# Kernel optimization log

Measured on AMD Instinct MI355X. Metric: run time of the kernel, lower is better.

Reference implementation:

```python
import jax, jax.numpy as jnp
import numpy as np

N, E, G = 50000, 1600000, 500
H, F, NG, L, OUT = 128, 128, 50, 6, 1
LOG2 = float(np.log(2.0))

def ssp(x):
    return jax.nn.softplus(x) - LOG2

def setup_inputs() -> dict:
    key = jax.random.key(0)
    ks = jax.random.split(key, 16)
    inp = {
        'z': jax.random.randint(ks[0], (N,), 0, 100),
        'pos': jax.random.normal(ks[1], (N, 3), jnp.float32) * 5.0,
        'batch': jnp.sort(jax.random.randint(ks[2], (N,), 0, G)),
        'edge_index': jax.random.randint(ks[3], (2, E), 0, N),
        # parameters
        'emb': jax.random.normal(ks[4], (100, H), jnp.float32) * 0.1,
        'dist_W': jax.random.normal(ks[5], (1, NG), jnp.float32) * 0.1,
        'dist_b': jnp.zeros((NG,), jnp.float32),
        'Wn': jax.random.normal(ks[6], (L, H, F), jnp.float32) * (1.0 / np.sqrt(H)),
        'We': jax.random.normal(ks[7], (L, NG, F), jnp.float32) * (1.0 / np.sqrt(NG)),
        'be': jnp.zeros((L, F), jnp.float32),
        'Wo': jax.random.normal(ks[8], (L, F, H), jnp.float32) * (1.0 / np.sqrt(F)),
        'bo': jnp.zeros((L, H), jnp.float32),
        'W1': jax.random.normal(ks[9], (H, H // 2), jnp.float32) * (1.0 / np.sqrt(H)),
        'b1': jnp.zeros((H // 2,), jnp.float32),
        'W2': jax.random.normal(ks[10], (H // 2, OUT), jnp.float32) * (1.0 / np.sqrt(H // 2)),
        'b2': jnp.zeros((OUT,), jnp.float32),
    }
    return inp

def reference(z, pos, batch, edge_index, emb, dist_W, dist_b, Wn, We, be, Wo, bo, W1, b1, W2, b2):
    row, col = edge_index[0], edge_index[1]
    # edge distances -> Linear(1, num_gaussians)
    dist = jnp.linalg.norm(pos[row] - pos[col], axis=-1)            # [E]
    e = dist[:, None] * dist_W[0][None, :] + dist_b                 # [E, NG]
    v = emb[z]                                                      # [N, H]
    # edge-conditioned message passing x num_layers
    for i in range(Wn.shape[0]):
        h = v @ Wn[i]                                               # [N, F]
        msg = h[col] * (e @ We[i] + be[i])                          # [E, F]
        agg = jax.ops.segment_sum(msg, row, num_segments=v.shape[0])
        v = ssp(agg @ Wo[i] + bo[i])                                # [N, H]
    # readout
    u = ssp(v @ W1 + b1) @ W2 + b2                                  # [N, OUT]
    return jax.ops.segment_sum(u, batch, num_segments=G)            # [G, OUT]
```

## Files before the change

kernel.cpp:

```cpp
#include <hip/hip_runtime.h>
#include <math.h>

#define HDIM 128
#define NGAUSS 50
#define NLAYER 6
#define TSTR 136
#define DINV (1.0f/512.0f)
#define NXCD 8
#define NSTRIPE 512

typedef unsigned short ushortT;
typedef __attribute__((ext_vector_type(8))) short bf16x8;
typedef __attribute__((ext_vector_type(4))) float f32x4;

static __device__ __forceinline__ float bf2f(unsigned short u){
  union { unsigned int i; float f; } x; x.i = ((unsigned int)u) << 16; return x.f;
}
static __device__ __forceinline__ float bitsf(unsigned int i){
  union { unsigned int i; float f; } x; x.i = i; return x.f;
}
static __device__ __forceinline__ unsigned short f2bf(float f){
  union { float f; unsigned int i; } x; x.f = f;
  unsigned int i = x.i;
  unsigned int r = (i + 0x7FFFu + ((i >> 16) & 1u)) >> 16;
  return (unsigned short)r;
}
static __device__ __forceinline__ float ssp(float x){
  return fmaxf(x, 0.0f) + __logf(1.0f + __expf(-fabsf(x))) - 0.69314718055994530942f;
}
static __device__ __forceinline__ f32x4 mfma4r(const bf16x8* a, const bf16x8* b){
  f32x4 d = {0.f, 0.f, 0.f, 0.f};
  d = __builtin_amdgcn_mfma_f32_16x16x32_bf16(a[0], b[0], d, 0, 0, 0);
  d = __builtin_amdgcn_mfma_f32_16x16x32_bf16(a[1], b[1], d, 0, 0, 0);
  d = __builtin_amdgcn_mfma_f32_16x16x32_bf16(a[2], b[2], d, 0, 0, 0);
  d = __builtin_amdgcn_mfma_f32_16x16x32_bf16(a[3], b[3], d, 0, 0, 0);
  return d;
}


__global__ __launch_bounds__(256)
void k_hist(const int* __restrict__ erow, int* __restrict__ hist,
            int E, int NB, int shift, int estripe){
  __shared__ int lh[512];
  int tid = threadIdx.x, w = blockIdx.x;
  for (int i = tid; i < NB; i += 256) lh[i] = 0;
  __syncthreads();
  int beg = w * estripe;
  int end = beg + estripe; if (end > E) end = E;
  for (int e = beg + tid; e < end; e += 256)
    atomicAdd(&lh[erow[e] >> shift], 1);
  __syncthreads();
  for (int i = tid; i < NB; i += 256) hist[w * 512 + i] = lh[i];
}

__global__ __launch_bounds__(256)
void k_colscan(int* __restrict__ hist, int* __restrict__ colTotal, int NB){
  __shared__ int sA[512], sB[512];
  int b = blockIdx.x, tid = threadIdx.x;
  sA[tid]       = hist[tid * 512 + b];
  sA[tid + 256] = hist[(tid + 256) * 512 + b];
  __syncthreads();
  int* pa = sA; int* pb = sB;
  for (int off = 1; off < 512; off <<= 1){
    for (int i = tid; i < 512; i += 256)
      pb[i] = pa[i] + (i >= off ? pa[i - off] : 0);
    __syncthreads();
    int* t = pa; pa = pb; pb = t;
  }
  int e0 = (tid == 0) ? 0 : pa[tid - 1];
  int e1 = pa[tid + 255];
  hist[tid * 512 + b]       = e0;
  hist[(tid + 256) * 512 + b] = e1;
  if (tid == 0) colTotal[b] = pa[511];
}

__global__ __launch_bounds__(256)
void k_bscan(const int* __restrict__ colTotal, int* __restrict__ bucketBase, int NB){
  __shared__ int sA[512], sB[512];
  int tid = threadIdx.x;
  for (int i = tid; i < 512; i += 256) sA[i] = (i < NB) ? colTotal[i] : 0;
  __syncthreads();
  int* pa = sA; int* pb = sB;
  for (int off = 1; off < 512; off <<= 1){
    for (int i = tid; i < 512; i += 256)
      pb[i] = pa[i] + (i >= off ? pa[i - off] : 0);
    __syncthreads();
    int* t = pa; pa = pb; pb = t;
  }
  for (int i = tid; i < NB; i += 256)
    bucketBase[i] = (i == 0) ? 0 : pa[i - 1];
  if (tid == 0) bucketBase[NB] = pa[NB - 1];
}

__global__ __launch_bounds__(256)
void k_scatter(const int* __restrict__ erow, const int* __restrict__ ecol,
               const float* __restrict__ pos, const int* __restrict__ hist,
               const int* __restrict__ bucketBase, uint2* __restrict__ stg,
               int E, int NB, int shift, int estripe){
  __shared__ int cur[512];
  int tid = threadIdx.x, w = blockIdx.x;
  for (int b = tid; b < NB; b += 256)
    cur[b] = bucketBase[b] + hist[w * 512 + b];
  __syncthreads();
  int beg = w * estripe;
  int end = beg + estripe; if (end > E) end = E;
  int mask = (1 << shift) - 1;
  for (int e = beg + tid; e < end; e += 256){
    int r = erow[e], c = ecol[e];
    float dx = pos[r*3+0] - pos[c*3+0];
    float dy = pos[r*3+1] - pos[c*3+1];
    float dz = pos[r*3+2] - pos[c*3+2];
    float d = sqrtf(dx*dx + dy*dy + dz*dz);
    int du = (int)(d * 512.0f + 0.5f);
    if (du > 65535) du = 65535;
    int p = atomicAdd(&cur[r >> shift], 1);
    uint2 t;
    t.x = ((unsigned int)c << 16) | (unsigned int)du;
    t.y = (unsigned int)(r & mask);
    stg[p] = t;
  }
}

__global__ __launch_bounds__(256)
void k_place(const uint2* __restrict__ stg, const int* __restrict__ bucketBase,
             int* __restrict__ offsets, unsigned int* __restrict__ csr,
             int N, int NB, int shift, int E){
  __shared__ int rc[1024];
  __shared__ int sA[1024], sB[1024];
  int b = blockIdx.x, tid = threadIdx.x;
  int R = 1 << shift;
  int r0 = b << shift;
  int s = bucketBase[b], e2 = bucketBase[b + 1];
  for (int i = tid; i < R; i += 256) rc[i] = 0;
  __syncthreads();
  for (int j = s + tid; j < e2; j += 256)
    atomicAdd(&rc[stg[j].y], 1);
  __syncthreads();
  for (int i = tid; i < R; i += 256) sA[i] = rc[i];
  __syncthreads();
  int* pa = sA; int* pb = sB;
  for (int off = 1; off < R; off <<= 1){
    for (int i = tid; i < R; i += 256)
      pb[i] = pa[i] + (i >= off ? pa[i - off] : 0);
    __syncthreads();
    int* t = pa; pa = pb; pb = t;
  }
  for (int i = tid; i < R; i += 256){
    int excl = (i == 0) ? 0 : pa[i - 1];
    rc[i] = excl;
    int r = r0 + i;
    if (r < N) offsets[r] = s + excl;
  }
  if (b == NB - 1 && tid == 0) offsets[N] = E;
  __syncthreads();
  for (int j = s + tid; j < e2; j += 256){
    uint2 t = stg[j];
    int slot = s + atomicAdd(&rc[t.y], 1);
    csr[slot] = t.x;
  }
}

__global__ void k_setup(const int* __restrict__ z, const float* __restrict__ emb,
                        ushortT* __restrict__ vhi,
                        const float* __restrict__ Wn, ushortT* __restrict__ WnT,
                        const float* __restrict__ Wo, ushortT* __restrict__ WoT,
                        const float* __restrict__ dW, const float* __restrict__ db,
                        const float* __restrict__ We, const float* __restrict__ be,
                        float* __restrict__ a, float* __restrict__ c,
                        const int* __restrict__ batch, int* __restrict__ groupOff,
                        const float* __restrict__ W1, ushortT* __restrict__ W1T,
                        int N, int G, int B1, int B2, int B4, int B5, int B7){
  int b = blockIdx.x;
  int tid = threadIdx.x;
  if (b < B1){
    int idx = b * 256 + tid;
    if (idx < N * HDIM){
      int n = idx >> 7, f = idx & 127;
      vhi[idx] = f2bf(emb[z[n] * HDIM + f]);
    }
    return;
  }
  b -= B1;
  if (b < B2){
    int idx = b * 256 + tid;
    if (idx < NLAYER * HDIM * HDIM){
      int mat = idx >> 14, rem = idx & 16383;
      int n = rem >> 7, k = rem & 127;
      WnT[idx] = f2bf(Wn[(mat << 14) + k * HDIM + n]);
    }
    return;
  }
  b -= B2;
  if (b < B2){
    int idx = b * 256 + tid;
    if (idx < NLAYER * HDIM * HDIM){
      int mat = idx >> 14, rem = idx & 16383;
      int n = rem >> 7, k = rem & 127;
      WoT[idx] = f2bf(Wo[(mat << 14) + k * HDIM + n]);
    }
    return;
  }
  b -= B2;
  if (b < B4){
    int idx = b * 256 + tid;
    if (idx < NLAYER * HDIM){
      int l = idx >> 7, f = idx & 127;
      float av = 0.f, cv = 0.f;
      for (int g = 0; g < NGAUSS; ++g){
        float we = We[(l * NGAUSS + g) * HDIM + f];
        av += dW[g] * we;
        cv += db[g] * we;
      }
      a[idx] = av;
      c[idx] = cv + be[idx];
    }
    return;
  }
  b -= B4;
  if (b < B5){
    int i = b * 256 + tid;
    if (i >= N) return;
    int bb = batch[i];
    if (i == 0){
      for (int g = 0; g <= bb; ++g) groupOff[g] = 0;
    } else {
      int pb = batch[i - 1];
      for (int g = pb + 1; g <= bb; ++g) groupOff[g] = i;
    }
    if (i == N - 1){
      for (int g = bb + 1; g <= G; ++g) groupOff[g] = N;
    }
    return;
  }
  b -= B5;
  if (b < B7){
    int idx = b * 256 + tid;
    if (idx < 64 * HDIM){
      int ncol = idx >> 7, k = idx & 127;
      W1T[idx] = f2bf(W1[k * 64 + ncol]);
    }
  }
}

__global__ __launch_bounds__(128, 2)
void k_gemm0(const ushortT* __restrict__ X, const ushortT* __restrict__ WT,
             ushortT* __restrict__ outHi, int N){
  int tid = threadIdx.x;
  int wave = tid >> 6, lane = tid & 63;
  int m = lane & 15, quad = lane >> 4;
  int ntiles = (N + 15) >> 4;
  int t0 = (blockIdx.x * 2 + wave) * 2;
  if (t0 >= ntiles) return;

  bf16x8 av[2][4];
  #pragma unroll
  for (int rt = 0; rt < 2; ++rt){
    int row = (t0 + rt) * 16 + m; if (row >= N) row = N - 1;
    #pragma unroll
    for (int kk = 0; kk < 4; ++kk)
      av[rt][kk] = *(const bf16x8*)(X + ((size_t)row << 7) + kk*32 + quad*8);
  }
  #pragma unroll
  for (int ct = 0; ct < 8; ++ct){
    int ncol = ct * 16 + m;
    const ushortT* bp = WT + ((size_t)ncol << 7) + quad*8;
    bf16x8 bb[4];
    #pragma unroll
    for (int kk = 0; kk < 4; ++kk) bb[kk] = *(const bf16x8*)(bp + kk*32);
    #pragma unroll
    for (int rt = 0; rt < 2; ++rt){
      f32x4 d = mfma4r(av[rt], bb);
      #pragma unroll
      for (int r = 0; r < 4; ++r){
        int orow = (t0 + rt) * 16 + quad*4 + r;
        if (orow < N) outHi[((size_t)orow << 7) + ncol] = f2bf(d[r]);
      }
    }
  }
}

#define AGG_PROC(P, DD) do { \
    unsigned int w_; float lo_, hi_; \
    w_ = (P).x; lo_ = bitsf(w_ << 16); hi_ = bitsf(w_ & 0xFFFF0000u); \
    s1[0] = fmaf(lo_, (DD), s1[0]); s0[0] += lo_; \
    s1[1] = fmaf(hi_, (DD), s1[1]); s0[1] += hi_; \
    w_ = (P).y; lo_ = bitsf(w_ << 16); hi_ = bitsf(w_ & 0xFFFF0000u); \
    s1[2] = fmaf(lo_, (DD), s1[2]); s0[2] += lo_; \
    s1[3] = fmaf(hi_, (DD), s1[3]); s0[3] += hi_; \
    w_ = (P).z; lo_ = bitsf(w_ << 16); hi_ = bitsf(w_ & 0xFFFF0000u); \
    s1[4] = fmaf(lo_, (DD), s1[4]); s0[4] += lo_; \
    s1[5] = fmaf(hi_, (DD), s1[5]); s0[5] += hi_; \
    w_ = (P).w; lo_ = bitsf(w_ << 16); hi_ = bitsf(w_ & 0xFFFF0000u); \
    s1[6] = fmaf(lo_, (DD), s1[6]); s0[6] += lo_; \
    s1[7] = fmaf(hi_, (DD), s1[7]); s0[7] += hi_; \
  } while(0)

#define GATH(Q) (*(const uint4*)(h + ((size_t)((Q) >> 16) << 7) + fl))

__global__ __launch_bounds__(256, 6)
void k_agg2(const ushortT* __restrict__ h, const int* __restrict__ offsets,
            const unsigned int* __restrict__ cd, const float* __restrict__ a,
            const float* __restrict__ c, ushortT* __restrict__ aggHi,
            int N, int segNodes){
  int xcd = blockIdx.x & (NXCD - 1);
  int idx = blockIdx.x >> 3;
  int node = xcd * segNodes + idx * 4 + (threadIdx.x >> 6);
  if (node >= N || node >= (xcd + 1) * segNodes) return;
  int lane = threadIdx.x & 63;
  int quarter = lane >> 4;
  int fl = (lane & 15) * 8;
  int s = offsets[node], e = offsets[node + 1];
  float s0[8] = {0.f,0.f,0.f,0.f,0.f,0.f,0.f,0.f};
  float s1[8] = {0.f,0.f,0.f,0.f,0.f,0.f,0.f,0.f};
  int efull = s + ((e - s) & ~7);
  int L = s;
  if (efull - s >= 16){
    unsigned int qA0 = cd[L + quarter],      qA1 = cd[L + 4 + quarter];
    uint4 pA0 = GATH(qA0), pA1 = GATH(qA1);
    unsigned int qB0 = cd[L + 8 + quarter],  qB1 = cd[L + 12 + quarter];
    uint4 pB0 = GATH(qB0), pB1 = GATH(qB1);
    float dA0 = (float)(qA0 & 0xFFFFu) * DINV, dA1 = (float)(qA1 & 0xFFFFu) * DINV;
    float dB0 = (float)(qB0 & 0xFFFFu) * DINV, dB1 = (float)(qB1 & 0xFFFFu) * DINV;
    L += 16;
    for (; L + 16 <= efull; L += 16){
      unsigned int nA0 = cd[L + quarter], nA1 = cd[L + 4 + quarter];
      AGG_PROC(pA0, dA0); AGG_PROC(pA1, dA1);
      pA0 = GATH(nA0); pA1 = GATH(nA1);
      dA0 = (float)(nA0 & 0xFFFFu) * DINV; dA1 = (float)(nA1 & 0xFFFFu) * DINV;
      unsigned int nB0 = cd[L + 8 + quarter], nB1 = cd[L + 12 + quarter];
      AGG_PROC(pB0, dB0); AGG_PROC(pB1, dB1);
      pB0 = GATH(nB0); pB1 = GATH(nB1);
      dB0 = (float)(nB0 & 0xFFFFu) * DINV; dB1 = (float)(nB1 & 0xFFFFu) * DINV;
    }
    AGG_PROC(pA0, dA0); AGG_PROC(pA1, dA1);
    AGG_PROC(pB0, dB0); AGG_PROC(pB1, dB1);
  }
  for (; L + 8 <= efull; L += 8){
    unsigned int q0 = cd[L + quarter], q1 = cd[L + 4 + quarter];
    uint4 p0 = GATH(q0), p1 = GATH(q1);
    float d0 = (float)(q0 & 0xFFFFu) * DINV, d1 = (float)(q1 & 0xFFFFu) * DINV;
    AGG_PROC(p0, d0); AGG_PROC(p1, d1);
  }
  for (int j = efull; j < e; j += 4){
    int myj = j + quarter;
    if (myj < e){
      unsigned int q = cd[myj];
      uint4 p = GATH(q);
      float dd = (float)(q & 0xFFFFu) * DINV;
      AGG_PROC(p, dd);
    }
  }
  float4 av0 = *(const float4*)(a + fl);
  float4 av1 = *(const float4*)(a + fl + 4);
  float4 cv0 = *(const float4*)(c + fl);
  float4 cv1 = *(const float4*)(c + fl + 4);
  float r[8];
  r[0] = av0.x * s1[0] + cv0.x * s0[0];
  r[1] = av0.y * s1[1] + cv0.y * s0[1];
  r[2] = av0.z * s1[2] + cv0.z * s0[2];
  r[3] = av0.w * s1[3] + cv0.w * s0[3];
  r[4] = av1.x * s1[4] + cv1.x * s0[4];
  r[5] = av1.y * s1[5] + cv1.y * s0[5];
  r[6] = av1.z * s1[6] + cv1.z * s0[6];
  r[7] = av1.w * s1[7] + cv1.w * s0[7];
  #pragma unroll
  for (int k = 0; k < 8; ++k){
    r[k] += __shfl_down(r[k], 32, 64);
    r[k] += __shfl_down(r[k], 16, 64);
  }
  if (quarter == 0){
    uint4 st;
    st.x = (unsigned int)f2bf(r[0]) | ((unsigned int)f2bf(r[1]) << 16);
    st.y = (unsigned int)f2bf(r[2]) | ((unsigned int)f2bf(r[3]) << 16);
    st.z = (unsigned int)f2bf(r[4]) | ((unsigned int)f2bf(r[5]) << 16);
    st.w = (unsigned int)f2bf(r[6]) | ((unsigned int)f2bf(r[7]) << 16);
    *(uint4*)(aggHi + ((size_t)node << 7) + fl) = st;
  }
}

__global__ __launch_bounds__(256, 2)
void k_fpair(const ushortT* __restrict__ agg, const ushortT* __restrict__ WoT,
             const float* __restrict__ bo, const ushortT* __restrict__ WnT,
             ushortT* __restrict__ outH, int N, int segTiles){
  __shared__ ushortT vt[2][32 * TSTR];
  int tid = threadIdx.x;
  int wave = tid >> 6, lane = tid & 63;
  int pairI = wave >> 1, half = wave & 1;
  int m = lane & 15, quad = lane >> 4;
  int ntiles = (N + 15) >> 4;
  int xcd = blockIdx.x & (NXCD - 1);
  int idx = blockIdx.x >> 3;
  int wjIdx = idx * 2 + pairI;
  int segWJ = segTiles >> 1;
  int t0 = xcd * segTiles + wjIdx * 2;
  bool act = (wjIdx < segWJ) && (t0 < ntiles);
  ushortT* vw = vt[pairI];

  bf16x8 av[2][4];
  if (act){
    #pragma unroll
    for (int rt = 0; rt < 2; ++rt){
      int row = (t0 + rt) * 16 + m; if (row >= N) row = N - 1;
      #pragma unroll
      for (int kk = 0; kk < 4; ++kk)
        av[rt][kk] = *(const bf16x8*)(agg + ((size_t)row << 7) + kk*32 + quad*8);
    }
    #pragma unroll
    for (int cti = 0; cti < 4; ++cti){
      int ncol = (half * 4 + cti) * 16 + m;
      const ushortT* bp = WoT + ((size_t)ncol << 7) + quad*8;
      bf16x8 bb[4];
      #pragma unroll
      for (int kk = 0; kk < 4; ++kk) bb[kk] = *(const bf16x8*)(bp + kk*32);
      float bbias = bo[ncol];
      #pragma unroll
      for (int rt = 0; rt < 2; ++rt){
        f32x4 d = mfma4r(av[rt], bb);
        #pragma unroll
        for (int r = 0; r < 4; ++r)
          vw[(rt*16 + quad*4 + r) * TSTR + ncol] = f2bf(ssp(d[r] + bbias));
      }
    }
  }
  __syncthreads();
  if (act){
    bf16x8 a2[2][4];
    #pragma unroll
    for (int rt = 0; rt < 2; ++rt){
      #pragma unroll
      for (int kk = 0; kk < 4; ++kk)
        a2[rt][kk] = *(const bf16x8*)(&vw[(rt*16 + m) * TSTR + kk*32 + quad*8]);
    }
    #pragma unroll
    for (int cti = 0; cti < 4; ++cti){
      int ncol = (half * 4 + cti) * 16 + m;
      const ushortT* bp = WnT + ((size_t)ncol << 7) + quad*8;
      bf16x8 bb[4];
      #pragma unroll
      for (int kk = 0; kk < 4; ++kk) bb[kk] = *(const bf16x8*)(bp + kk*32);
      #pragma unroll
      for (int rt = 0; rt < 2; ++rt){
        f32x4 d = mfma4r(a2[rt], bb);
        #pragma unroll
        for (int r = 0; r < 4; ++r){
          int orow = (t0 + rt) * 16 + quad*4 + r;
          if (orow < N) outH[((size_t)orow << 7) + ncol] = f2bf(d[r]);
        }
      }
    }
  }
}

__global__ __launch_bounds__(256, 2)
void k_gfinal(const ushortT* __restrict__ agg, const ushortT* __restrict__ WoT,
              const float* __restrict__ bo, const ushortT* __restrict__ W1T,
              const float* __restrict__ b1, const float* __restrict__ W2,
              const float* __restrict__ b2, float* __restrict__ u,
              int N, int segTiles){
  __shared__ ushortT vt[2][32 * TSTR];
  __shared__ float part[2][2][32];
  int tid = threadIdx.x;
  int wave = tid >> 6, lane = tid & 63;
  int pairI = wave >> 1, half = wave & 1;
  int m = lane & 15, quad = lane >> 4;
  int ntiles = (N + 15) >> 4;
  int xcd = blockIdx.x & (NXCD - 1);
  int idx = blockIdx.x >> 3;
  int wjIdx = idx * 2 + pairI;
  int segWJ = segTiles >> 1;
  int t0 = xcd * segTiles + wjIdx * 2;
  bool act = (wjIdx < segWJ) && (t0 < ntiles);
  ushortT* vw = vt[pairI];

  if (act){
    bf16x8 av[2][4];
    #pragma unroll
    for (int rt = 0; rt < 2; ++rt){
      int row = (t0 + rt) * 16 + m; if (row >= N) row = N - 1;
      #pragma unroll
      for (int kk = 0; kk < 4; ++kk)
        av[rt][kk] = *(const bf16x8*)(agg + ((size_t)row << 7) + kk*32 + quad*8);
    }
    #pragma unroll
    for (int cti = 0; cti < 4; ++cti){
      int ncol = (half * 4 + cti) * 16 + m;
      const ushortT* bp = WoT + ((size_t)ncol << 7) + quad*8;
      bf16x8 bb[4];
      #pragma unroll
      for (int kk = 0; kk < 4; ++kk) bb[kk] = *(const bf16x8*)(bp + kk*32);
      float bbias = bo[ncol];
      #pragma unroll
      for (int rt = 0; rt < 2; ++rt){
        f32x4 d = mfma4r(av[rt], bb);
        #pragma unroll
        for (int r = 0; r < 4; ++r)
          vw[(rt*16 + quad*4 + r) * TSTR + ncol] = f2bf(ssp(d[r] + bbias));
      }
    }
  }
  __syncthreads();
  if (act){
    bf16x8 a2[2][4];
    #pragma unroll
    for (int rt = 0; rt < 2; ++rt){
      #pragma unroll
      for (int kk = 0; kk < 4; ++kk)
        a2[rt][kk] = *(const bf16x8*)(&vw[(rt*16 + m) * TSTR + kk*32 + quad*8]);
    }
    float acc[2][4] = {{0.f,0.f,0.f,0.f},{0.f,0.f,0.f,0.f}};
    #pragma unroll
    for (int cti = 0; cti < 2; ++cti){
      int ncol = (half * 2 + cti) * 16 + m;
      const ushortT* bp = W1T + ((size_t)ncol << 7) + quad*8;
      bf16x8 bb[4];
      #pragma unroll
      for (int kk = 0; kk < 4; ++kk) bb[kk] = *(const bf16x8*)(bp + kk*32);
      float bb1 = b1[ncol];
      float w2  = W2[ncol];
      #pragma unroll
      for (int rt = 0; rt < 2; ++rt){
        f32x4 d = mfma4r(a2[rt], bb);
        #pragma unroll
        for (int r = 0; r < 4; ++r)
          acc[rt][r] += ssp(d[r] + bb1) * w2;
      }
    }
    #pragma unroll
    for (int rt = 0; rt < 2; ++rt){
      #pragma unroll
      for (int r = 0; r < 4; ++r){
        float v = acc[rt][r];
        v += __shfl_xor(v, 1, 64);
        v += __shfl_xor(v, 2, 64);
        v += __shfl_xor(v, 4, 64);
        v += __shfl_xor(v, 8, 64);
        if (m == 0) part[pairI][half][rt*16 + quad*4 + r] = v;
      }
    }
  }
  __syncthreads();
  if (tid < 64){
    int p = tid >> 5, row = tid & 31;
    int wj = idx * 2 + p;
    int tt = xcd * segTiles + wj * 2;
    if (wj < segWJ && tt < ntiles){
      int orow = tt * 16 + row;
      if (orow < N) u[orow] = part[p][0][row] + part[p][1][row] + b2[0];
    }
  }
}

__global__ void k_gsum(const float* __restrict__ u, const int* __restrict__ groupOff,
                       float* __restrict__ out, int G){
  int g = blockIdx.x * 4 + (threadIdx.x >> 6);
  if (g >= G) return;
  int lane = threadIdx.x & 63;
  int s = groupOff[g], e = groupOff[g + 1];
  float acc = 0.f;
  for (int j = s + lane; j < e; j += 64) acc += u[j];
  #pragma unroll
  for (int off = 32; off > 0; off >>= 1)
    acc += __shfl_down(acc, off, 64);
  if (lane == 0) out[g] = acc;
}

extern "C" void kernel_launch(void* const* d_in, const int* in_sizes, int n_in,
                              void* d_out, int out_size, void* d_ws, size_t ws_size,
                              hipStream_t stream){
  const int N = in_sizes[0];
  const int E = in_sizes[3] / 2;
  const int G = out_size;

  const int*   z     = (const int*)d_in[0];
  const float* pos   = (const float*)d_in[1];
  const int*   batch = (const int*)d_in[2];
  const int*   eidx  = (const int*)d_in[3];
  const int*   erow  = eidx;
  const int*   ecol  = eidx + E;
  const float* emb   = (const float*)d_in[4];
  const float* dW    = (const float*)d_in[5];
  const float* db    = (const float*)d_in[6];
  const float* Wn    = (const float*)d_in[7];
  const float* We    = (const float*)d_in[8];
  const float* be    = (const float*)d_in[9];
  const float* Wo    = (const float*)d_in[10];
  const float* bo    = (const float*)d_in[11];
  const float* W1    = (const float*)d_in[12];
  const float* b1    = (const float*)d_in[13];
  const float* W2    = (const float*)d_in[14];
  const float* b2    = (const float*)d_in[15];

  char* ws = (char*)d_ws;
  size_t off = 0;
  auto alloc = [&](size_t bytes) -> char* {
    char* p = ws + off;
    off = (off + bytes + 255) & ~(size_t)255;
    return p;
  };
  size_t hbytes = (size_t)N * HDIM * 2;
  size_t stgbytes = (size_t)E * 8;
  int*          offsets  = (int*)         alloc((size_t)(N + 1) * 4);
  unsigned int* csr      = (unsigned int*)alloc((size_t)E * 4);
  ushortT*      h0       = (ushortT*)     alloc(hbytes);
  ushortT*      h1       = (ushortT*)     alloc(hbytes);
  ushortT*      vhi      = (ushortT*)     alloc(hbytes);
  ushortT*      agghi    = (ushortT*)     alloc(hbytes);
  ushortT*      stgbuf   = (ushortT*)     alloc(stgbytes);
  ushortT*      WnT      = (ushortT*)     alloc((size_t)NLAYER * HDIM * HDIM * 2);
  ushortT*      WoT      = (ushortT*)     alloc((size_t)NLAYER * HDIM * HDIM * 2);
  ushortT*      W1T      = (ushortT*)     alloc((size_t)64 * HDIM * 2);
  float*        a        = (float*)       alloc((size_t)NLAYER * HDIM * 4);
  float*        c        = (float*)       alloc((size_t)NLAYER * HDIM * 4);
  float*        u        = (float*)       alloc((size_t)N * 4);
  int*          groupOff = (int*)         alloc((size_t)(G + 1) * 4);

  int*   hist       = (int*)h1;
  int*   colTotal   = hist + NSTRIPE * 512;
  int*   bucketBase = colTotal + 512;
  uint2* stg        = (uint2*)stgbuf;

  int shift = 7;
  while ((((N - 1) >> shift) + 1) > 512) ++shift;
  int NB = ((N - 1) >> shift) + 1;
  int estripe = (E + NSTRIPE - 1) / NSTRIPE;

  int B1 = (N * HDIM + 255) / 256;
  int B2 = (NLAYER * HDIM * HDIM + 255) / 256;
  int B4 = (NLAYER * HDIM + 255) / 256;
  int B5 = (N + 255) / 256;
  int B7 = (64 * HDIM + 255) / 256;
  k_setup<<<B1 + 2*B2 + B4 + B5 + B7, 256, 0, stream>>>(
      z, emb, vhi, Wn, WnT, Wo, WoT,
      dW, db, We, be, a, c, batch, groupOff, W1, W1T,
      N, G, B1, B2, B4, B5, B7);

  k_hist   <<<NSTRIPE, 256, 0, stream>>>(erow, hist, E, NB, shift, estripe);
  k_colscan<<<NB,      256, 0, stream>>>(hist, colTotal, NB);
  k_bscan  <<<1,       256, 0, stream>>>(colTotal, bucketBase, NB);
  k_scatter<<<NSTRIPE, 256, 0, stream>>>(erow, ecol, pos, hist, bucketBase,
                                         stg, E, NB, shift, estripe);
  k_place  <<<NB,      256, 0, stream>>>(stg, bucketBase, offsets, csr, N, NB, shift, E);

  int ntiles = (N + 15) >> 4;
  int segTiles = (((ntiles + NXCD - 1) / NXCD) + 1) & ~1;
  int segNodes = segTiles * 16;
  int segWJ = segTiles >> 1;
  int aggGrid  = NXCD * ((segNodes + 3) / 4);
  int gGrid    = NXCD * ((segWJ + 1) / 2);
  int nwj = (ntiles + 1) / 2;
  int pairGrid = (nwj + 1) / 2;
  k_gemm0<<<pairGrid, 128, 0, stream>>>(vhi, WnT, h0, N);

  for (int l = 0; l < NLAYER; ++l){
    size_t wo = (size_t)l * HDIM * HDIM;
    const ushortT* hin  = (l & 1) ? h1 : h0;
    ushortT*       hout = (l & 1) ? h0 : h1;
    k_agg2<<<aggGrid, 256, 0, stream>>>(hin, offsets, csr,
                                        a + l * HDIM, c + l * HDIM, agghi, N, segNodes);
    if (l < NLAYER - 1){
      size_t wn = (size_t)(l + 1) * HDIM * HDIM;
      k_fpair<<<gGrid, 256, 0, stream>>>(agghi, WoT + wo, bo + (size_t)l * HDIM,
                                         WnT + wn, hout, N, segTiles);
    } else {
      k_gfinal<<<gGrid, 256, 0, stream>>>(agghi, WoT + wo, bo + (size_t)l * HDIM,
                                          W1T, b1, W2, b2, u, N, segTiles);
    }
  }
  k_gsum<<<(G + 3) / 4, 256, 0, stream>>>(u, groupOff, (float*)d_out, G);
}
```

Before: 582.5 us.

## Precompute embedding times Wn0 table, fuse histogram into setup, pack agg FMAs

The first-layer node projection is now computed once on a 100-row embedding table (emb@Wn[0]) and gathered per node, which removes the N×128×128 gemm0 kernel and the vhi buffer. The edge histogram kernel is folded into k_setup as extra blocks, saving a launch. The aggregation inner loop switches to 2-wide float vectors so the compiler can emit packed FMA/add instructions. The new path also rounds emb@Wn to bf16 in a slightly different order, which risks small numeric differences.

```diff
diff --git a/kernel.cpp b/kernel.cpp
--- a/kernel.cpp
+++ b/kernel.cpp
@@ -12,6 +12,7 @@
 typedef unsigned short ushortT;
 typedef __attribute__((ext_vector_type(8))) short bf16x8;
 typedef __attribute__((ext_vector_type(4))) float f32x4;
+typedef __attribute__((ext_vector_type(2))) float f32x2;
 
 static __device__ __forceinline__ float bf2f(unsigned short u){
   union { unsigned int i; float f; } x; x.i = ((unsigned int)u) << 16; return x.f;
@@ -37,21 +38,6 @@
   return d;
 }
 
-
-__global__ __launch_bounds__(256)
-void k_hist(const int* __restrict__ erow, int* __restrict__ hist,
-            int E, int NB, int shift, int estripe){
-  __shared__ int lh[512];
-  int tid = threadIdx.x, w = blockIdx.x;
-  for (int i = tid; i < NB; i += 256) lh[i] = 0;
-  __syncthreads();
-  int beg = w * estripe;
-  int end = beg + estripe; if (end > E) end = E;
-  for (int e = beg + tid; e < end; e += 256)
-    atomicAdd(&lh[erow[e] >> shift], 1);
-  __syncthreads();
-  for (int i = tid; i < NB; i += 256) hist[w * 512 + i] = lh[i];
-}
 
 __global__ __launch_bounds__(256)
 void k_colscan(int* __restrict__ hist, int* __restrict__ colTotal, int NB){
@@ -160,8 +146,21 @@
   }
 }
 
-__global__ void k_setup(const int* __restrict__ z, const float* __restrict__ emb,
-                        ushortT* __restrict__ vhi,
+__global__ __launch_bounds__(256)
+void k_emb2(const float* __restrict__ emb, const float* __restrict__ Wn,
+            ushortT* __restrict__ emb2){
+  int idx = blockIdx.x * 256 + threadIdx.x;
+  if (idx >= 100 * HDIM) return;
+  int i = idx >> 7, f = idx & 127;
+  float acc = 0.f;
+  #pragma unroll 8
+  for (int k = 0; k < HDIM; ++k)
+    acc = fmaf(emb[i * HDIM + k], Wn[k * HDIM + f], acc);
+  emb2[idx] = f2bf(acc);
+}
+
+__global__ void k_setup(const int* __restrict__ z, const ushortT* __restrict__ emb2,
+                        ushortT* __restrict__ h0,
                         const float* __restrict__ Wn, ushortT* __restrict__ WnT,
                         const float* __restrict__ Wo, ushortT* __restrict__ WoT,
                         const float* __restrict__ dW, const float* __restrict__ db,
@@ -169,14 +168,17 @@
                         float* __restrict__ a, float* __restrict__ c,
                         const int* __restrict__ batch, int* __restrict__ groupOff,
                         const float* __restrict__ W1, ushortT* __restrict__ W1T,
-                        int N, int G, int B1, int B2, int B4, int B5, int B7){
+                        const int* __restrict__ erow, int* __restrict__ hist,
+                        int N, int G, int E, int estripe, int NB, int shift,
+                        int B1, int B2, int B4, int B5, int B7){
+  __shared__ int lh[512];
   int b = blockIdx.x;
   int tid = threadIdx.x;
   if (b < B1){
     int idx = b * 256 + tid;
     if (idx < N * HDIM){
       int n = idx >> 7, f = idx & 127;
-      vhi[idx] = f2bf(emb[z[n] * HDIM + f]);
+      h0[idx] = emb2[z[n] * HDIM + f];
     }
     return;
   }
@@ -239,60 +241,32 @@
       int ncol = idx >> 7, k = idx & 127;
       W1T[idx] = f2bf(W1[k * 64 + ncol]);
     }
-  }
-}
-
-__global__ __launch_bounds__(128, 2)
-void k_gemm0(const ushortT* __restrict__ X, const ushortT* __restrict__ WT,
-             ushortT* __restrict__ outHi, int N){
-  int tid = threadIdx.x;
-  int wave = tid >> 6, lane = tid & 63;
-  int m = lane & 15, quad = lane >> 4;
-  int ntiles = (N + 15) >> 4;
-  int t0 = (blockIdx.x * 2 + wave) * 2;
-  if (t0 >= ntiles) return;
-
-  bf16x8 av[2][4];
-  #pragma unroll
-  for (int rt = 0; rt < 2; ++rt){
-    int row = (t0 + rt) * 16 + m; if (row >= N) row = N - 1;
-    #pragma unroll
-    for (int kk = 0; kk < 4; ++kk)
-      av[rt][kk] = *(const bf16x8*)(X + ((size_t)row << 7) + kk*32 + quad*8);
-  }
-  #pragma unroll
-  for (int ct = 0; ct < 8; ++ct){
-    int ncol = ct * 16 + m;
-    const ushortT* bp = WT + ((size_t)ncol << 7) + quad*8;
-    bf16x8 bb[4];
-    #pragma unroll
-    for (int kk = 0; kk < 4; ++kk) bb[kk] = *(const bf16x8*)(bp + kk*32);
-    #pragma unroll
-    for (int rt = 0; rt < 2; ++rt){
-      f32x4 d = mfma4r(av[rt], bb);
-      #pragma unroll
-      for (int r = 0; r < 4; ++r){
-        int orow = (t0 + rt) * 16 + quad*4 + r;
-        if (orow < N) outHi[((size_t)orow << 7) + ncol] = f2bf(d[r]);
-      }
-    }
-  }
-}
-
-#define AGG_PROC(P, DD) do { \
-    unsigned int w_; float lo_, hi_; \
-    w_ = (P).x; lo_ = bitsf(w_ << 16); hi_ = bitsf(w_ & 0xFFFF0000u); \
-    s1[0] = fmaf(lo_, (DD), s1[0]); s0[0] += lo_; \
-    s1[1] = fmaf(hi_, (DD), s1[1]); s0[1] += hi_; \
-    w_ = (P).y; lo_ = bitsf(w_ << 16); hi_ = bitsf(w_ & 0xFFFF0000u); \
-    s1[2] = fmaf(lo_, (DD), s1[2]); s0[2] += lo_; \
-    s1[3] = fmaf(hi_, (DD), s1[3]); s0[3] += hi_; \
-    w_ = (P).z; lo_ = bitsf(w_ << 16); hi_ = bitsf(w_ & 0xFFFF0000u); \
-    s1[4] = fmaf(lo_, (DD), s1[4]); s0[4] += lo_; \
-    s1[5] = fmaf(hi_, (DD), s1[5]); s0[5] += hi_; \
-    w_ = (P).w; lo_ = bitsf(w_ << 16); hi_ = bitsf(w_ & 0xFFFF0000u); \
-    s1[6] = fmaf(lo_, (DD), s1[6]); s0[6] += lo_; \
-    s1[7] = fmaf(hi_, (DD), s1[7]); s0[7] += hi_; \
+    return;
+  }
+  b -= B7;
+  if (b < NSTRIPE){
+    for (int i = tid; i < NB; i += 256) lh[i] = 0;
+    __syncthreads();
+    int beg = b * estripe;
+    int end = beg + estripe; if (end > E) end = E;
+    for (int e = beg + tid; e < end; e += 256)
+      atomicAdd(&lh[erow[e] >> shift], 1);
+    __syncthreads();
+    for (int i = tid; i < NB; i += 256) hist[b * 512 + i] = lh[i];
+  }
+}
+
+#define SPLAT(x) (f32x2){(x),(x)}
+#define AGG_PROC(P, DDV) do { \
+    unsigned int w_; f32x2 hv_; \
+    w_ = (P).x; hv_.x = bitsf(w_ << 16); hv_.y = bitsf(w_ & 0xFFFF0000u); \
+    s1v0 = __builtin_elementwise_fma(hv_, (DDV), s1v0); s0v0 += hv_; \
+    w_ = (P).y; hv_.x = bitsf(w_ << 16); hv_.y = bitsf(w_ & 0xFFFF0000u); \
+    s1v1 = __builtin_elementwise_fma(hv_, (DDV), s1v1); s0v1 += hv_; \
+    w_ = (P).z; hv_.x = bitsf(w_ << 16); hv_.y = bitsf(w_ & 0xFFFF0000u); \
+    s1v2 = __builtin_elementwise_fma(hv_, (DDV), s1v2); s0v2 += hv_; \
+    w_ = (P).w; hv_.x = bitsf(w_ << 16); hv_.y = bitsf(w_ & 0xFFFF0000u); \
+    s1v3 = __builtin_elementwise_fma(hv_, (DDV), s1v3); s0v3 += hv_; \
   } while(0)
 
 #define GATH(Q) (*(const uint4*)(h + ((size_t)((Q) >> 16) << 7) + fl))
@@ -310,8 +284,8 @@
   int quarter = lane >> 4;
   int fl = (lane & 15) * 8;
   int s = offsets[node], e = offsets[node + 1];
-  float s0[8] = {0.f,0.f,0.f,0.f,0.f,0.f,0.f,0.f};
-  float s1[8] = {0.f,0.f,0.f,0.f,0.f,0.f,0.f,0.f};
+  f32x2 s0v0 = {0.f,0.f}, s0v1 = {0.f,0.f}, s0v2 = {0.f,0.f}, s0v3 = {0.f,0.f};
+  f32x2 s1v0 = {0.f,0.f}, s1v1 = {0.f,0.f}, s1v2 = {0.f,0.f}, s1v3 = {0.f,0.f};
   int efull = s + ((e - s) & ~7);
   int L = s;
   if (efull - s >= 16){
@@ -319,18 +293,22 @@
     uint4 pA0 = GATH(qA0), pA1 = GATH(qA1);
     unsigned int qB0 = cd[L + 8 + quarter],  qB1 = cd[L + 12 + quarter];
     uint4 pB0 = GATH(qB0), pB1 = GATH(qB1);
-    float dA0 = (float)(qA0 & 0xFFFFu) * DINV, dA1 = (float)(qA1 & 0xFFFFu) * DINV;
-    float dB0 = (float)(qB0 & 0xFFFFu) * DINV, dB1 = (float)(qB1 & 0xFFFFu) * DINV;
+    f32x2 dA0 = SPLAT((float)(qA0 & 0xFFFFu) * DINV);
+    f32x2 dA1 = SPLAT((float)(qA1 & 0xFFFFu) * DINV);
+    f32x2 dB0 = SPLAT((float)(qB0 & 0xFFFFu) * DINV);
+    f32x2 dB1 = SPLAT((float)(qB1 & 0xFFFFu) * DINV);
     L += 16;
     for (; L + 16 <= efull; L += 16){
       unsigned int nA0 = cd[L + quarter], nA1 = cd[L + 4 + quarter];
       AGG_PROC(pA0, dA0); AGG_PROC(pA1, dA1);
       pA0 = GATH(nA0); pA1 = GATH(nA1);
-      dA0 = (float)(nA0 & 0xFFFFu) * DINV; dA1 = (float)(nA1 & 0xFFFFu) * DINV;
+      dA0 = SPLAT((float)(nA0 & 0xFFFFu) * DINV);
+      dA1 = SPLAT((float)(nA1 & 0xFFFFu) * DINV);
       unsigned int nB0 = cd[L + 8 + quarter], nB1 = cd[L + 12 + quarter];
       AGG_PROC(pB0, dB0); AGG_PROC(pB1, dB1);
       pB0 = GATH(nB0); pB1 = GATH(nB1);
-      dB0 = (float)(nB0 & 0xFFFFu) * DINV; dB1 = (float)(nB1 & 0xFFFFu) * DINV;
+      dB0 = SPLAT((float)(nB0 & 0xFFFFu) * DINV);
+      dB1 = SPLAT((float)(nB1 & 0xFFFFu) * DINV);
     }
     AGG_PROC(pA0, dA0); AGG_PROC(pA1, dA1);
     AGG_PROC(pB0, dB0); AGG_PROC(pB1, dB1);
@@ -338,7 +316,8 @@
   for (; L + 8 <= efull; L += 8){
     unsigned int q0 = cd[L + quarter], q1 = cd[L + 4 + quarter];
     uint4 p0 = GATH(q0), p1 = GATH(q1);
-    float d0 = (float)(q0 & 0xFFFFu) * DINV, d1 = (float)(q1 & 0xFFFFu) * DINV;
+    f32x2 d0 = SPLAT((float)(q0 & 0xFFFFu) * DINV);
+    f32x2 d1 = SPLAT((float)(q1 & 0xFFFFu) * DINV);
     AGG_PROC(p0, d0); AGG_PROC(p1, d1);
   }
   for (int j = efull; j < e; j += 4){
@@ -346,7 +325,7 @@
     if (myj < e){
       unsigned int q = cd[myj];
       uint4 p = GATH(q);
-      float dd = (float)(q & 0xFFFFu) * DINV;
+      f32x2 dd = SPLAT((float)(q & 0xFFFFu) * DINV);
       AGG_PROC(p, dd);
     }
   }
@@ -355,14 +334,14 @@
   float4 cv0 = *(const float4*)(c + fl);
   float4 cv1 = *(const float4*)(c + fl + 4);
   float r[8];
-  r[0] = av0.x * s1[0] + cv0.x * s0[0];
-  r[1] = av0.y * s1[1] + cv0.y * s0[1];
-  r[2] = av0.z * s1[2] + cv0.z * s0[2];
-  r[3] = av0.w * s1[3] + cv0.w * s0[3];
-  r[4] = av1.x * s1[4] + cv1.x * s0[4];
-  r[5] = av1.y * s1[5] + cv1.y * s0[5];
-  r[6] = av1.z * s1[6] + cv1.z * s0[6];
-  r[7] = av1.w * s1[7] + cv1.w * s0[7];
+  r[0] = av0.x * s1v0.x + cv0.x * s0v0.x;
+  r[1] = av0.y * s1v0.y + cv0.y * s0v0.y;
+  r[2] = av0.z * s1v1.x + cv0.z * s0v1.x;
+  r[3] = av0.w * s1v1.y + cv0.w * s0v1.y;
+  r[4] = av1.x * s1v2.x + cv1.x * s0v2.x;
+  r[5] = av1.y * s1v2.y + cv1.y * s0v2.y;
+  r[6] = av1.z * s1v3.x + cv1.z * s0v3.x;
+  r[7] = av1.w * s1v3.y + cv1.w * s0v3.y;
   #pragma unroll
   for (int k = 0; k < 8; ++k){
     r[k] += __shfl_down(r[k], 32, 64);
@@ -603,9 +582,9 @@
   unsigned int* csr      = (unsigned int*)alloc((size_t)E * 4);
   ushortT*      h0       = (ushortT*)     alloc(hbytes);
   ushortT*      h1       = (ushortT*)     alloc(hbytes);
-  ushortT*      vhi      = (ushortT*)     alloc(hbytes);
   ushortT*      agghi    = (ushortT*)     alloc(hbytes);
   ushortT*      stgbuf   = (ushortT*)     alloc(stgbytes);
+  ushortT*      emb2     = (ushortT*)     alloc((size_t)100 * HDIM * 2);
   ushortT*      WnT      = (ushortT*)     alloc((size_t)NLAYER * HDIM * HDIM * 2);
   ushortT*      WoT      = (ushortT*)     alloc((size_t)NLAYER * HDIM * HDIM * 2);
   ushortT*      W1T      = (ushortT*)     alloc((size_t)64 * HDIM * 2);
@@ -629,12 +608,14 @@
   int B4 = (NLAYER * HDIM + 255) / 256;
   int B5 = (N + 255) / 256;
   int B7 = (64 * HDIM + 255) / 256;
-  k_setup<<<B1 + 2*B2 + B4 + B5 + B7, 256, 0, stream>>>(
-      z, emb, vhi, Wn, WnT, Wo, WoT,
+
+  k_emb2<<<(100 * HDIM + 255) / 256, 256, 0, stream>>>(emb, Wn, emb2);
+  k_setup<<<B1 + 2*B2 + B4 + B5 + B7 + NSTRIPE, 256, 0, stream>>>(
+      z, emb2, h0, Wn, WnT, Wo, WoT,
       dW, db, We, be, a, c, batch, groupOff, W1, W1T,
-      N, G, B1, B2, B4, B5, B7);
-
-  k_hist   <<<NSTRIPE, 256, 0, stream>>>(erow, hist, E, NB, shift, estripe);
+      erow, hist,
+      N, G, E, estripe, NB, shift, B1, B2, B4, B5, B7);
+
   k_colscan<<<NB,      256, 0, stream>>>(hist, colTotal, NB);
   k_bscan  <<<1,       256, 0, stream>>>(colTotal, bucketBase, NB);
   k_scatter<<<NSTRIPE, 256, 0, stream>>>(erow, ecol, pos, hist, bucketBase,
@@ -647,9 +628,6 @@
   int segWJ = segTiles >> 1;
   int aggGrid  = NXCD * ((segNodes + 3) / 4);
   int gGrid    = NXCD * ((segWJ + 1) / 2);
-  int nwj = (ntiles + 1) / 2;
-  int pairGrid = (nwj + 1) / 2;
-  k_gemm0<<<pairGrid, 128, 0, stream>>>(vhi, WnT, h0, N);
 
   for (int l = 0; l < NLAYER; ++l){
     size_t wo = (size_t)l * HDIM * HDIM;
```

New measurement: 608.8 us. 4.5% more time.
